# Performance work log

Hardware: AMD Instinct MI355X
Metric: run time of the kernel (lower is better)

The kernel has to match this reference:

```python
import jax, jax.numpy as jnp
import numpy as np

H = 1024      # hidden_size
V = 32000     # vocab (len(dictionary)) for both src and tgt
T_IN = 64     # input_length
T_OUT = 64    # target_length (teacher forcing -> static)
BOS = 0

_PARAM_NAMES = [
    "enc_Wih0", "enc_Whh0", "enc_bih0", "enc_bhh0",
    "enc_Wih1", "enc_Whh1", "enc_bih1", "enc_bhh1",
    "dec_Wih0", "dec_Whh0", "dec_bih0", "dec_bhh0",
    "dec_Wih1", "dec_Whh1", "dec_bih1", "dec_bhh1",
]


def setup_inputs() -> dict:
    key = jax.random.key(0)
    ks = jax.random.split(key, 32)

    def p(k, shape):
        return jax.random.normal(k, shape, dtype=jnp.float32) * 0.02

    inp = {
        "src_tokens": jax.random.randint(ks[0], (T_IN,), 0, V),
        # targets in [0, V-1) so EOS (= V-1) never appears -> fixed-length loop is faithful
        "tgt_tokens": jax.random.randint(ks[1], (T_OUT,), 0, V - 1),
        "emb_src": p(ks[2], (V, H)),
        "emb_tgt": p(ks[3], (V, H)),
    }
    i = 4
    for n in _PARAM_NAMES:
        shape = (4 * H, H) if "W" in n else (4 * H,)
        inp[n] = p(ks[i], shape)
        i += 1
    inp["out_W"] = p(ks[i], (V, H))
    inp["out_b"] = jnp.zeros((V,), jnp.float32)
    return inp


def _cell(x, h, c, Wih, Whh, bih, bhh):
    # PyTorch LSTM cell, gate order i, f, g, o
    g = x @ Wih.T + h @ Whh.T + bih + bhh
    i_, f_, g_, o_ = jnp.split(g, 4, axis=-1)
    c2 = jax.nn.sigmoid(f_) * c + jax.nn.sigmoid(i_) * jnp.tanh(g_)
    h2 = jax.nn.sigmoid(o_) * jnp.tanh(c2)
    return h2, c2


def _run_lstm2(emb, carry, params):
    # 2-layer LSTM scanned over time; emb: (T, H); carry: (h0, c0, h1, c1) each (H,)
    Wih0, Whh0, bih0, bhh0, Wih1, Whh1, bih1, bhh1 = params

    def step(carry, x):
        h0, c0, h1, c1 = carry
        h0, c0 = _cell(x, h0, c0, Wih0, Whh0, bih0, bhh0)
        h1, c1 = _cell(h0, h1, c1, Wih1, Whh1, bih1, bhh1)
        return (h0, c0, h1, c1), h1

    return jax.lax.scan(step, carry, emb)


def _forward(src_tokens, tgt_tokens, emb_src, emb_tgt, enc_params, dec_params, out_W, out_b):
    z = jnp.zeros((H,), jnp.float32)
    # encoder: token-by-token LSTM; final (h, c) seeds the decoder
    carry, _enc_hs = _run_lstm2(emb_src[src_tokens], (z, z, z, z), enc_params)
    # decoder, teacher forcing: input at step t is BOS then target[t-1]
    dec_in = jnp.concatenate([jnp.array([BOS], dtype=tgt_tokens.dtype), tgt_tokens[:-1]])
    _, dec_h = _run_lstm2(emb_tgt[dec_in], carry, dec_params)  # (T_OUT, H)
    logits = jax.nn.relu(dec_h) @ out_W.T + out_b  # (T_OUT, V)
    return logits[:, None, :]  # torch.stack of (1, V) outputs -> (T_OUT, 1, V)


def reference(src_tokens, tgt_tokens, emb_src, emb_tgt,
              enc_Wih0, enc_Whh0, enc_bih0, enc_bhh0,
              enc_Wih1, enc_Whh1, enc_bih1, enc_bhh1,
              dec_Wih0, dec_Whh0, dec_bih0, dec_bhh0,
              dec_Wih1, dec_Whh1, dec_bih1, dec_bhh1,
              out_W, out_b):
    enc_params = (enc_Wih0, enc_Whh0, enc_bih0, enc_bhh0,
                  enc_Wih1, enc_Whh1, enc_bih1, enc_bhh1)
    dec_params = (dec_Wih0, dec_Whh0, dec_bih0, dec_bhh0,
                  dec_Wih1, dec_Whh1, dec_bih1, dec_bhh1)
    return _forward(src_tokens, tgt_tokens, emb_src, emb_tgt,
                    enc_params, dec_params, out_W, out_b)
```

## Files before the change

### kernel.cpp

```cpp
#include <hip/hip_runtime.h>
#include <cstdint>
#include <cstddef>


#define NH   1024
#define NG   4096
#define NT   64
#define NV   32000
#define NWG  256
#define NTHR 256

struct SeqParams {
  const int *src, *tgt;
  const float *emb_src, *emb_tgt;
  const float *eWih0, *eWhh0, *ebih0, *ebhh0;
  const float *eWih1, *eWhh1, *ebih1, *ebhh1;
  const float *dWih0, *dWhh0, *dbih0, *dbhh0;
  const float *dWih1, *dWhh1, *dbih1, *dbhh1;
  const float *outW, *outb;
  float *out;
  unsigned *cnt;
  unsigned *flag;
  unsigned *gcnt;
  float *h0b, *h1b, *gihE, *gihD, *dechT;
};

__device__ __forceinline__ float sigf(float x) { return 1.f / (1.f + expf(-x)); }

template <bool FENCED>
__device__ __forceinline__ void gbar(const SeqParams& p, unsigned round) {
  __syncthreads();
  if (threadIdx.x == 0) {
    if (FENCED) __threadfence();
    unsigned* gc = p.gcnt + ((blockIdx.x >> 5) << 5);
    unsigned gprev = __hip_atomic_fetch_add(gc, 1u, __ATOMIC_RELAXED,
                                            __HIP_MEMORY_SCOPE_AGENT);
    bool released = false;
    if (gprev == round * 32u - 1u) {
      unsigned rprev = __hip_atomic_fetch_add(p.cnt, 1u, __ATOMIC_RELAXED,
                                              __HIP_MEMORY_SCOPE_AGENT);
      if (rprev == round * 8u - 1u) {
        __hip_atomic_store(p.flag, round, __ATOMIC_RELAXED, __HIP_MEMORY_SCOPE_AGENT);
        released = true;
      }
    }
    if (!released) {
      for (unsigned it = 0; it < 8000000u; ++it) {
        if (__hip_atomic_load(p.flag, __ATOMIC_RELAXED, __HIP_MEMORY_SCOPE_AGENT)
            >= round) break;
        __builtin_amdgcn_s_sleep(1);
      }
    }
    if (FENCED) __threadfence();
  }
  __syncthreads();
}

__device__ __forceinline__ void load_row64(const float* base, float* dst, int c16) {
  const float4* s = (const float4*)base + c16;
  #pragma unroll
  for (int i = 0; i < 16; ++i) {
    float4 v = s[16*i];
    dst[4*i+0]=v.x; dst[4*i+1]=v.y; dst[4*i+2]=v.z; dst[4*i+3]=v.w;
  }
}

__global__ __launch_bounds__(NTHR, 1)
void seq2seq_kernel(SeqParams p) {
  const int tid = threadIdx.x;
  const int wg  = blockIdx.x;
  const int gt  = wg * NTHR + tid;
  const int u   = gt >> 6;
  const int l   = gt & 63;
  const int gi  = l >> 4;
  const int c16 = l & 15;
  const int rowg = gi * NH + u;
  unsigned rnd = 0;

  __shared__ float Wl[32 * NH];
  float* hst0 = Wl;
  float* hst1 = Wl + NH;

  for (int half = 0; half < 2; ++half) {
    const float* W   = half ? p.dWih0 : p.eWih0;
    const float* bi  = half ? p.dbih0 : p.ebih0;
    const float* bh  = half ? p.dbhh0 : p.ebhh0;
    const float* emb = half ? p.emb_tgt : p.emb_src;
    float* gih       = half ? p.gihD : p.gihE;
    for (int pp = 0; pp < 4; ++pp) {
      int pair = pp * NTHR + tid;
      int row  = wg * 16 + (pair >> 6);
      int t    = pair & 63;
      int tok  = half ? (t ? p.tgt[t-1] : 0) : p.src[t];
      const float4* xr = (const float4*)(emb + (size_t)tok * NH);
      const float4* wr = (const float4*)(W + (size_t)row * NH);
      float a0=0.f,a1=0.f,a2=0.f,a3=0.f;
      #pragma unroll 4
      for (int k = 0; k < NH/4; ++k) {
        float4 x = xr[k], w = wr[k];
        a0 = fmaf(x.x,w.x,a0); a1 = fmaf(x.y,w.y,a1);
        a2 = fmaf(x.z,w.z,a2); a3 = fmaf(x.w,w.w,a3);
      }
      gih[t*NG + row] = (a0+a1)+(a2+a3) + bi[row] + bh[row];
    }
  }

  float w0[64], wiA[64], whA[64];
  load_row64(p.eWhh0 + (size_t)rowg*NH, w0,  c16);
  load_row64(p.eWih1 + (size_t)rowg*NH, wiA, c16);
  load_row64(p.eWhh1 + (size_t)rowg*NH, whA, c16);
  float b1 = p.ebih1[rowg] + p.ebhh1[rowg];

  float c0s = 0.f, c1s = 0.f;

  gbar<true>(p, ++rnd);

  for (int phase = 0; phase < 2; ++phase) {
    const float* gih = phase ? p.gihD : p.gihE;
    for (int r = 0; r <= NT; ++r) {
      float gval = (r < NT) ? gih[r*NG + rowg] : 0.f;
      {
        const float* hb0 = p.h0b + (((r&1)^1) << 10);
        const float* hb1 = p.h1b + ((r&1) << 10);
        #pragma unroll
        for (int j = 0; j < 4; ++j) {
          hst0[j*256 + tid] = __hip_atomic_load(hb0 + j*256 + tid,
                                 __ATOMIC_RELAXED, __HIP_MEMORY_SCOPE_AGENT);
          hst1[j*256 + tid] = __hip_atomic_load(hb1 + j*256 + tid,
                                 __ATOMIC_RELAXED, __HIP_MEMORY_SCOPE_AGENT);
        }
      }
      __syncthreads();

      float h0s[64];
      load_row64(hst0, h0s, c16);

      if (r < NT) {
        float a0=0.f,a1=0.f,a2=0.f,a3=0.f;
        #pragma unroll
        for (int i = 0; i < 16; ++i) {
          a0 = fmaf(w0[4*i+0], h0s[4*i+0], a0);
          a1 = fmaf(w0[4*i+1], h0s[4*i+1], a1);
          a2 = fmaf(w0[4*i+2], h0s[4*i+2], a2);
          a3 = fmaf(w0[4*i+3], h0s[4*i+3], a3);
        }
        float acc = (a0+a1)+(a2+a3);
        #pragma unroll
        for (int m = 1; m <= 8; m <<= 1) acc += __shfl_xor(acc, m, 64);
        acc += gval;
        float p0 = __shfl(acc, c16,      64);
        float p1 = __shfl(acc, c16 + 16, 64);
        float p2 = __shfl(acc, c16 + 32, 64);
        float p3 = __shfl(acc, c16 + 48, 64);
        c0s = sigf(p1) * c0s + sigf(p0) * tanhf(p2);
        float h0new = sigf(p3) * tanhf(c0s);
        if (l == 0)
          __hip_atomic_store(&p.h0b[((r&1) << 10) + u], h0new,
                             __ATOMIC_RELAXED, __HIP_MEMORY_SCOPE_AGENT);
      }

      if (r >= 1) {
        float h1s[64];
        load_row64(hst1, h1s, c16);
        float a0=0.f,a1=0.f,a2=0.f,a3=0.f;
        #pragma unroll
        for (int i = 0; i < 16; ++i) {
          a0 = fmaf(wiA[4*i+0], h0s[4*i+0], a0);
          a1 = fmaf(wiA[4*i+1], h0s[4*i+1], a1);
          a2 = fmaf(wiA[4*i+2], h0s[4*i+2], a2);
          a3 = fmaf(wiA[4*i+3], h0s[4*i+3], a3);
        }
        #pragma unroll
        for (int i = 0; i < 16; ++i) {
          a0 = fmaf(whA[4*i+0], h1s[4*i+0], a0);
          a1 = fmaf(whA[4*i+1], h1s[4*i+1], a1);
          a2 = fmaf(whA[4*i+2], h1s[4*i+2], a2);
          a3 = fmaf(whA[4*i+3], h1s[4*i+3], a3);
        }
        float acc = (a0+a1)+(a2+a3);
        #pragma unroll
        for (int m = 1; m <= 8; m <<= 1) acc += __shfl_xor(acc, m, 64);
        acc += b1;
        float p0 = __shfl(acc, c16,      64);
        float p1 = __shfl(acc, c16 + 16, 64);
        float p2 = __shfl(acc, c16 + 32, 64);
        float p3 = __shfl(acc, c16 + 48, 64);
        c1s = sigf(p1) * c1s + sigf(p0) * tanhf(p2);
        float h1new = sigf(p3) * tanhf(c1s);
        if (l == 0) {
          __hip_atomic_store(&p.h1b[(((r&1)^1) << 10) + u], h1new,
                             __ATOMIC_RELAXED, __HIP_MEMORY_SCOPE_AGENT);
          if (phase) {
            int tt = r - 1;
            p.dechT[(u >> 2)*256 + tt*4 + (u & 3)] = fmaxf(h1new, 0.f);
          }
        }
      }
      if (phase == 1 && r == NT) gbar<true>(p, ++rnd);
      else                       gbar<false>(p, ++rnd);
    }
    if (phase == 0) {
      load_row64(p.dWhh0 + (size_t)rowg*NH, w0,  c16);
      load_row64(p.dWih1 + (size_t)rowg*NH, wiA, c16);
      load_row64(p.dWhh1 + (size_t)rowg*NH, whA, c16);
      b1 = p.dbih1[rowg] + p.dbhh1[rowg];
    }
  }

  const int t  = tid & 63;
  const int vs = tid >> 6;
  const int vbase = wg * 125;
  const float4* xT4 = (const float4*)p.dechT;
  float4* Wl4 = (float4*)Wl;
  const float4* oW4 = (const float4*)p.outW;
  for (int ch = 0; ch < 4; ++ch) {
    int rbase = ch * 32;
    __syncthreads();
    #pragma unroll
    for (int i = 0; i < 32; ++i) {
      int vr = rbase + i; if (vr > 124) vr = 124;
      Wl4[i*256 + tid] = oW4[(size_t)(vbase + vr)*256 + tid];
    }
    __syncthreads();
    float ac[32];
    #pragma unroll
    for (int i = 0; i < 32; ++i) ac[i] = 0.f;
    const float4* q0 = (const float4*)(Wl + (8*vs+0)*NH);
    const float4* q1 = (const float4*)(Wl + (8*vs+1)*NH);
    const float4* q2 = (const float4*)(Wl + (8*vs+2)*NH);
    const float4* q3 = (const float4*)(Wl + (8*vs+3)*NH);
    const float4* q4 = (const float4*)(Wl + (8*vs+4)*NH);
    const float4* q5 = (const float4*)(Wl + (8*vs+5)*NH);
    const float4* q6 = (const float4*)(Wl + (8*vs+6)*NH);
    const float4* q7 = (const float4*)(Wl + (8*vs+7)*NH);
    #pragma unroll 4
    for (int kb = 0; kb < 256; ++kb) {
      float4 x = xT4[kb*64 + t];
      float4 w;
      w = q0[kb]; ac[ 0]=fmaf(x.x,w.x,ac[ 0]); ac[ 1]=fmaf(x.y,w.y,ac[ 1]); ac[ 2]=fmaf(x.z,w.z,ac[ 2]); ac[ 3]=fmaf(x.w,w.w,ac[ 3]);
      w = q1[kb]; ac[ 4]=fmaf(x.x,w.x,ac[ 4]); ac[ 5]=fmaf(x.y,w.y,ac[ 5]); ac[ 6]=fmaf(x.z,w.z,ac[ 6]); ac[ 7]=fmaf(x.w,w.w,ac[ 7]);
      w = q2[kb]; ac[ 8]=fmaf(x.x,w.x,ac[ 8]); ac[ 9]=fmaf(x.y,w.y,ac[ 9]); ac[10]=fmaf(x.z,w.z,ac[10]); ac[11]=fmaf(x.w,w.w,ac[11]);
      w = q3[kb]; ac[12]=fmaf(x.x,w.x,ac[12]); ac[13]=fmaf(x.y,w.y,ac[13]); ac[14]=fmaf(x.z,w.z,ac[14]); ac[15]=fmaf(x.w,w.w,ac[15]);
      w = q4[kb]; ac[16]=fmaf(x.x,w.x,ac[16]); ac[17]=fmaf(x.y,w.y,ac[17]); ac[18]=fmaf(x.z,w.z,ac[18]); ac[19]=fmaf(x.w,w.w,ac[19]);
      w = q5[kb]; ac[20]=fmaf(x.x,w.x,ac[20]); ac[21]=fmaf(x.y,w.y,ac[21]); ac[22]=fmaf(x.z,w.z,ac[22]); ac[23]=fmaf(x.w,w.w,ac[23]);
      w = q6[kb]; ac[24]=fmaf(x.x,w.x,ac[24]); ac[25]=fmaf(x.y,w.y,ac[25]); ac[26]=fmaf(x.z,w.z,ac[26]); ac[27]=fmaf(x.w,w.w,ac[27]);
      w = q7[kb]; ac[28]=fmaf(x.x,w.x,ac[28]); ac[29]=fmaf(x.y,w.y,ac[29]); ac[30]=fmaf(x.z,w.z,ac[30]); ac[31]=fmaf(x.w,w.w,ac[31]);
    }
    #pragma unroll
    for (int j = 0; j < 8; ++j) {
      int cr = rbase + 8*vs + j;
      if (cr < 125) {
        int v = vbase + cr;
        float s = (ac[4*j]+ac[4*j+1])+(ac[4*j+2]+ac[4*j+3]);
        p.out[(size_t)t*NV + v] = s + p.outb[v];
      }
    }
  }
}

extern "C" void kernel_launch(void* const* d_in, const int* in_sizes, int n_in,
                              void* d_out, int out_size, void* d_ws, size_t ws_size,
                              hipStream_t stream) {
  (void)in_sizes; (void)n_in; (void)out_size; (void)ws_size;
  SeqParams P;
  P.src     = (const int*)d_in[0];
  P.tgt     = (const int*)d_in[1];
  P.emb_src = (const float*)d_in[2];
  P.emb_tgt = (const float*)d_in[3];
  P.eWih0 = (const float*)d_in[4];  P.eWhh0 = (const float*)d_in[5];
  P.ebih0 = (const float*)d_in[6];  P.ebhh0 = (const float*)d_in[7];
  P.eWih1 = (const float*)d_in[8];  P.eWhh1 = (const float*)d_in[9];
  P.ebih1 = (const float*)d_in[10]; P.ebhh1 = (const float*)d_in[11];
  P.dWih0 = (const float*)d_in[12]; P.dWhh0 = (const float*)d_in[13];
  P.dbih0 = (const float*)d_in[14]; P.dbhh0 = (const float*)d_in[15];
  P.dWih1 = (const float*)d_in[16]; P.dWhh1 = (const float*)d_in[17];
  P.dbih1 = (const float*)d_in[18]; P.dbhh1 = (const float*)d_in[19];
  P.outW  = (const float*)d_in[20];
  P.outb  = (const float*)d_in[21];
  P.out   = (float*)d_out;

  char* ws = (char*)d_ws;
  P.cnt   = (unsigned*)ws;
  P.flag  = (unsigned*)(ws + 256);
  P.gcnt  = (unsigned*)(ws + 512);
  P.h0b   = (float*)(ws + 2048);
  P.h1b   = (float*)(ws + 10240);
  P.gihE  = (float*)(ws + 18432);
  P.gihD  = (float*)(ws + 18432 + 1048576);
  P.dechT = (float*)(ws + 18432 + 2097152);
  hipMemsetAsync(d_ws, 0, 18432, stream);

  seq2seq_kernel<<<dim3(NWG), dim3(NTHR), 0, stream>>>(P);
}
```

Before: 1.605 ms.

## Use master-block flag barrier and replicate hidden-state buffers across 16 copies

Replaces the hierarchical atomic-counter grid barrier with a scheme where each block writes its own padded slot and block 0 polls all slots in parallel, then broadcasts release through 16 replicated flags. Hidden state vectors h0/h1 are also written to 16 replicas so that groups of workgroups read from different memory locations, spreading the contention on shared L2 lines. This is meant to cut per-step barrier latency and read hot-spotting in the 130-round recurrent loop, at the cost of more stores per step and a larger workspace memset.

```diff
diff --git a/kernel.cpp b/kernel.cpp
--- a/kernel.cpp
+++ b/kernel.cpp
@@ -9,6 +9,7 @@
 #define NV   32000
 #define NWG  256
 #define NTHR 256
+#define NREP 16
 
 struct SeqParams {
   const int *src, *tgt;
@@ -19,10 +20,10 @@
   const float *dWih1, *dWhh1, *dbih1, *dbhh1;
   const float *outW, *outb;
   float *out;
-  unsigned *cnt;
+  unsigned *slot;
   unsigned *flag;
-  unsigned *gcnt;
-  float *h0b, *h1b, *gihE, *gihD, *dechT;
+  float *h0b, *h1b;
+  float *gihE, *gihD, *dechT;
 };
 
 __device__ __forceinline__ float sigf(float x) { return 1.f / (1.f + expf(-x)); }
@@ -30,30 +31,36 @@
 template <bool FENCED>
 __device__ __forceinline__ void gbar(const SeqParams& p, unsigned round) {
   __syncthreads();
-  if (threadIdx.x == 0) {
-    if (FENCED) __threadfence();
-    unsigned* gc = p.gcnt + ((blockIdx.x >> 5) << 5);
-    unsigned gprev = __hip_atomic_fetch_add(gc, 1u, __ATOMIC_RELAXED,
-                                            __HIP_MEMORY_SCOPE_AGENT);
-    bool released = false;
-    if (gprev == round * 32u - 1u) {
-      unsigned rprev = __hip_atomic_fetch_add(p.cnt, 1u, __ATOMIC_RELAXED,
-                                              __HIP_MEMORY_SCOPE_AGENT);
-      if (rprev == round * 8u - 1u) {
-        __hip_atomic_store(p.flag, round, __ATOMIC_RELAXED, __HIP_MEMORY_SCOPE_AGENT);
-        released = true;
-      }
-    }
-    if (!released) {
+  const int tid = threadIdx.x;
+  if (blockIdx.x == 0) {
+    if (FENCED && tid == 0) __threadfence();
+    for (unsigned it = 0; it < 8000000u; ++it) {
+      unsigned v = (tid == 0) ? round
+          : __hip_atomic_load(p.slot + tid * 32, __ATOMIC_RELAXED,
+                              __HIP_MEMORY_SCOPE_AGENT);
+      if (__syncthreads_and((int)(v >= round))) break;
+      __builtin_amdgcn_s_sleep(1);
+    }
+    if (tid < 16)
+      __hip_atomic_store(p.flag + tid * 32, round, __ATOMIC_RELAXED,
+                         __HIP_MEMORY_SCOPE_AGENT);
+    if (FENCED && tid == 0) __threadfence();
+    __syncthreads();
+  } else {
+    if (tid == 0) {
+      if (FENCED) __threadfence();
+      __hip_atomic_store(p.slot + blockIdx.x * 32, round, __ATOMIC_RELAXED,
+                         __HIP_MEMORY_SCOPE_AGENT);
+      const unsigned fi = (blockIdx.x & 15) * 32;
       for (unsigned it = 0; it < 8000000u; ++it) {
-        if (__hip_atomic_load(p.flag, __ATOMIC_RELAXED, __HIP_MEMORY_SCOPE_AGENT)
-            >= round) break;
+        if (__hip_atomic_load(p.flag + fi, __ATOMIC_RELAXED,
+                              __HIP_MEMORY_SCOPE_AGENT) >= round) break;
         __builtin_amdgcn_s_sleep(1);
       }
-    }
-    if (FENCED) __threadfence();
-  }
-  __syncthreads();
+      if (FENCED) __threadfence();
+    }
+    __syncthreads();
+  }
 }
 
 __device__ __forceinline__ void load_row64(const float* base, float* dst, int c16) {
@@ -120,8 +127,8 @@
     for (int r = 0; r <= NT; ++r) {
       float gval = (r < NT) ? gih[r*NG + rowg] : 0.f;
       {
-        const float* hb0 = p.h0b + (((r&1)^1) << 10);
-        const float* hb1 = p.h1b + ((r&1) << 10);
+        const float* hb0 = p.h0b + ((((wg & 15) << 1) | ((r & 1) ^ 1)) << 10);
+        const float* hb1 = p.h1b + ((((wg & 15) << 1) | (r & 1)) << 10);
         #pragma unroll
         for (int j = 0; j < 4; ++j) {
           hst0[j*256 + tid] = __hip_atomic_load(hb0 + j*256 + tid,
@@ -154,8 +161,8 @@
         float p3 = __shfl(acc, c16 + 48, 64);
         c0s = sigf(p1) * c0s + sigf(p0) * tanhf(p2);
         float h0new = sigf(p3) * tanhf(c0s);
-        if (l == 0)
-          __hip_atomic_store(&p.h0b[((r&1) << 10) + u], h0new,
+        if (l < NREP)
+          __hip_atomic_store(p.h0b + (((l << 1) | (r & 1)) << 10) + u, h0new,
                              __ATOMIC_RELAXED, __HIP_MEMORY_SCOPE_AGENT);
       }
 
@@ -187,13 +194,12 @@
         float p3 = __shfl(acc, c16 + 48, 64);
         c1s = sigf(p1) * c1s + sigf(p0) * tanhf(p2);
         float h1new = sigf(p3) * tanhf(c1s);
-        if (l == 0) {
-          __hip_atomic_store(&p.h1b[(((r&1)^1) << 10) + u], h1new,
+        if (l < NREP)
+          __hip_atomic_store(p.h1b + (((l << 1) | ((r & 1) ^ 1)) << 10) + u, h1new,
                              __ATOMIC_RELAXED, __HIP_MEMORY_SCOPE_AGENT);
-          if (phase) {
-            int tt = r - 1;
-            p.dechT[(u >> 2)*256 + tt*4 + (u & 3)] = fmaxf(h1new, 0.f);
-          }
+        if (l == 0 && phase) {
+          int tt = r - 1;
+          p.dechT[(u >> 2)*256 + tt*4 + (u & 3)] = fmaxf(h1new, 0.f);
         }
       }
       if (phase == 1 && r == NT) gbar<true>(p, ++rnd);
@@ -280,15 +286,14 @@
   P.out   = (float*)d_out;
 
   char* ws = (char*)d_ws;
-  P.cnt   = (unsigned*)ws;
-  P.flag  = (unsigned*)(ws + 256);
-  P.gcnt  = (unsigned*)(ws + 512);
-  P.h0b   = (float*)(ws + 2048);
-  P.h1b   = (float*)(ws + 10240);
-  P.gihE  = (float*)(ws + 18432);
-  P.gihD  = (float*)(ws + 18432 + 1048576);
-  P.dechT = (float*)(ws + 18432 + 2097152);
-  hipMemsetAsync(d_ws, 0, 18432, stream);
+  P.slot  = (unsigned*)ws;
+  P.flag  = (unsigned*)(ws + 32768);
+  P.h0b   = (float*)(ws + 34816);
+  P.h1b   = (float*)(ws + 165888);
+  P.gihE  = (float*)(ws + 296960);
+  P.gihD  = (float*)(ws + 296960 + 1048576);
+  P.dechT = (float*)(ws + 296960 + 2097152);
+  hipMemsetAsync(d_ws, 0, 296960, stream);
 
   seq2seq_kernel<<<dim3(NWG), dim3(NTHR), 0, stream>>>(P);
 }
```

New measurement: 1.610 ms. No clear change (+0.3%).
